# Performance work log

Hardware: AMD Instinct MI355X
Metric: run time of the kernel (lower is better)

## Reference

```python
import jax, jax.numpy as jnp
import numpy as np


def setup_inputs() -> dict:
    key = jax.random.key(0)
    x = jax.random.normal(key, (8192, 32768), dtype=jnp.float32)
    return {"x": x, "k": 64}


def reference(x, k):
    # ReLU then keep only top-k values per row; everything else zeroed.
    x_relu = jax.nn.relu(x)
    kk = min(k, x.shape[-1])
    vals, idx = jax.lax.top_k(x_relu, kk)            # [B, k]
    rows = jnp.arange(x.shape[0])[:, None]           # [B, 1]
    out = jnp.zeros_like(x).at[rows, idx].set(vals)
    return out
```

## Files before the change

### kernel.cpp

```cpp
#include <hip/hip_runtime.h>
#include <stdint.h>


#define NT   1024
#define NCOL 32768
#define VPT  8
#define NB   2048
#define REP  2
#define LISTCAP 2048

__global__ __launch_bounds__(NT) void topk_select_kernel(
        const float* __restrict__ x, const int* __restrict__ kptr,
        float* __restrict__ out)
{
    __shared__ uint32_t hist[REP][NB];
    __shared__ uint32_t tielist[LISTCAP];
    __shared__ int s_found, s_B, s_kth, s_neq, s_cnt, s_cut;

    const int tid  = threadIdx.x;
    const int lane = tid & 63;
    const int wave = tid >> 6;
    const size_t base = (size_t)blockIdx.x * NCOL;

    int k = *kptr;
    if (k > NCOL) k = NCOL;

    const uint4* xv = (const uint4*)(x + base);
    uint4*       ov = (uint4*)(out + base);

    if (k <= 0) {
        #pragma unroll
        for (int j = 0; j < VPT; ++j)
            ov[j * NT + tid] = make_uint4(0u, 0u, 0u, 0u);
        return;
    }

    uint4 va[VPT];
    #pragma unroll
    for (int j = 0; j < VPT; ++j) va[j] = xv[j * NT + tid];
    #pragma unroll
    for (int j = 0; j < VPT; ++j) {
        uint32_t* p = (uint32_t*)&va[j];
        #pragma unroll
        for (int c = 0; c < 4; ++c) {
            uint32_t u = p[c];
            p[c] = ((int)u > 0) ? u : 0u;
        }
    }

    int kth = k;
    uint32_t prefix = 0u;
    uint32_t thr = 0u;
    int n_eq = 0;
    bool done = false;

    #pragma unroll
    for (int round = 0; round < 3; ++round) {
        for (int i = tid; i < REP * NB; i += NT)
            ((uint32_t*)hist)[i] = 0u;
        __syncthreads();

        if (!done) {
            const int r = wave & (REP - 1);
            #pragma unroll
            for (int j = 0; j < VPT; ++j) {
                const uint32_t* p = (const uint32_t*)&va[j];
                #pragma unroll
                for (int c = 0; c < 4; ++c) {
                    uint32_t vv = p[c];
                    bool act; uint32_t bin;
                    if (round == 0)      { act = (vv != 0u);                          bin = vv >> 21; }
                    else if (round == 1) { act = (vv != 0u) && ((vv >> 21) == prefix); bin = (vv >> 10) & 0x7FFu; }
                    else                 { act = (vv != 0u) && ((vv >> 10) == prefix); bin = vv & 0x3FFu; }
                    if (act) atomicAdd(&hist[r][bin], 1u);
                }
            }
        }
        __syncthreads();

        if (wave == 0) {
            uint32_t s = 0;
            for (int i = 0; i < 32; ++i) {
                int b = lane * 32 + ((i + lane) & 31);
                #pragma unroll
                for (int r2 = 0; r2 < REP; ++r2) s += hist[r2][b];
            }
            uint32_t suf = s;
            #pragma unroll
            for (int d = 1; d < 64; d <<= 1) {
                uint32_t t2 = __shfl_down(suf, d);
                if (lane + d < 64) suf += t2;
            }
            uint32_t t1  = __shfl_down(suf, 1);
            uint32_t nxt = (lane == 63) ? 0u : t1;
            bool cond = (!done) && (suf >= (uint32_t)kth) && (nxt < (uint32_t)kth);
            unsigned long long mask = __ballot(cond);
            if (mask == 0ull) {
                if (lane == 0) s_found = 0;
            } else {
                int G = __ffsll(mask) - 1;
                uint32_t cntG = __shfl(nxt, G);
                uint32_t h2 = 0;
                if (lane < 32) {
                    int b = G * 32 + lane;
                    #pragma unroll
                    for (int r2 = 0; r2 < REP; ++r2) h2 += hist[r2][b];
                }
                uint32_t suf2 = h2;
                #pragma unroll
                for (int d = 1; d < 64; d <<= 1) {
                    uint32_t t2 = __shfl_down(suf2, d);
                    if (lane + d < 64) suf2 += t2;
                }
                uint32_t t3   = __shfl_down(suf2, 1);
                uint32_t nxt2 = (lane == 63) ? 0u : t3;
                uint32_t ts   = cntG + suf2;
                uint32_t tsn  = cntG + nxt2;
                bool cond2 = (lane < 32) && (ts >= (uint32_t)kth) && (tsn < (uint32_t)kth);
                unsigned long long m2 = __ballot(cond2);
                int l = __ffsll(m2) - 1;
                uint32_t ngt  = __shfl(tsn, l);
                uint32_t cbin = __shfl(suf2 - nxt2, l);
                if (lane == 0) {
                    s_found = 1;
                    s_B   = G * 32 + l;
                    s_kth = kth - (int)ngt;
                    s_neq = (int)cbin;
                }
            }
        }
        __syncthreads();

        if (!done) {
            if (!s_found) { done = true; thr = 0u; }
            else {
                int B = s_B;
                kth  = s_kth;
                n_eq = s_neq;
                if (round == 0)      prefix = (uint32_t)B;
                else if (round == 1) prefix = (prefix << 11) | (uint32_t)B;
                else                 thr    = (prefix << 10) | (uint32_t)B;
            }
        }
        __syncthreads();
    }

    if (tid == 0) s_cnt = 0;
    __syncthreads();
    const bool need_tb = (thr != 0u) && (n_eq != kth);
    if (need_tb) {
        #pragma unroll
        for (int j = 0; j < VPT; ++j) {
            const uint32_t* p = (const uint32_t*)&va[j];
            #pragma unroll
            for (int c = 0; c < 4; ++c) {
                if (p[c] == thr) {
                    int slot = atomicAdd(&s_cnt, 1);
                    if (slot < LISTCAP)
                        tielist[slot] = (uint32_t)(j * 4096 + tid * 4 + c);
                }
            }
        }
    }
    __syncthreads();
    if (need_tb && tid == 0) {
        int n = s_cnt; if (n > LISTCAP) n = LISTCAP;
        for (int i = 1; i < n; ++i) {
            uint32_t key = tielist[i]; int j2 = i - 1;
            while (j2 >= 0 && tielist[j2] > key) { tielist[j2 + 1] = tielist[j2]; --j2; }
            tielist[j2 + 1] = key;
        }
        s_cut = (kth >= 1 && kth <= n) ? (int)tielist[kth - 1] : 0x7FFFFFFF;
    }
    __syncthreads();
    const int idx_cut = need_tb ? s_cut : 0x7FFFFFFF;

    #pragma unroll
    for (int j = 0; j < VPT; ++j) {
        const uint32_t* p = (const uint32_t*)&va[j];
        uint4 o;
        uint32_t* q = (uint32_t*)&o;
        #pragma unroll
        for (int c = 0; c < 4; ++c) {
            uint32_t vv = p[c];
            int idx = j * 4096 + tid * 4 + c;
            bool keep = (vv > thr) || (thr != 0u && vv == thr && idx <= idx_cut);
            q[c] = keep ? vv : 0u;
        }
        ov[j * NT + tid] = o;
    }
}

extern "C" void kernel_launch(void* const* d_in, const int* in_sizes, int n_in,
                              void* d_out, int out_size, void* d_ws, size_t ws_size,
                              hipStream_t stream) {
    const float* x    = (const float*)d_in[0];
    const int*   kptr = (const int*)d_in[1];
    float*       out  = (float*)d_out;
    const int rows = in_sizes[0] / NCOL;
    topk_select_kernel<<<rows, NT, 0, stream>>>(x, kptr, out);
}
```

Before: 1.767 ms.

## Early-exit radix select via small candidate list with parallel rank selection

Stops the radix histogram rounds as soon as the bin holding the k-th value has at most 1024 elements. Those candidates (value plus reversed index) are gathered into shared memory and the exact k-th element is found with a parallel O(n^2) rank count. Histogram replicas are interleaved four-way to cut atomic contention, and output vectors with no value in the top bin are zero-stored early. The aim is to skip later histogram passes and the serial insertion-sort tie-break, at the cost of more branches and a quadratic rank loop over up to 1024 candidates.

```diff
diff --git a/kernel.cpp b/kernel.cpp
--- a/kernel.cpp
+++ b/kernel.cpp
@@ -2,20 +2,23 @@
 #include <stdint.h>
 
 
-#define NT   1024
-#define NCOL 32768
-#define VPT  8
-#define NB   2048
-#define REP  2
-#define LISTCAP 2048
+#define NT    1024
+#define NCOL  32768
+#define VPT   8
+#define NB    2048
+#define REP   4
+#define CAP   1024
 
 __global__ __launch_bounds__(NT) void topk_select_kernel(
         const float* __restrict__ x, const int* __restrict__ kptr,
         float* __restrict__ out)
 {
-    __shared__ uint32_t hist[REP][NB];
-    __shared__ uint32_t tielist[LISTCAP];
-    __shared__ int s_found, s_B, s_kth, s_neq, s_cnt, s_cut;
+    __shared__ uint32_t hist[NB][REP];
+    __shared__ uint32_t red[NB];
+    __shared__ uint64_t cand[CAP];
+    __shared__ int s_found, s_B, s_kth, s_cnt, s_nc;
+    __shared__ uint32_t s_thr;
+    __shared__ int s_cut;
 
     const int tid  = threadIdx.x;
     const int lane = tid & 63;
@@ -47,34 +50,76 @@
             p[c] = ((int)u > 0) ? u : 0u;
         }
     }
+    if (tid == 0) s_nc = 0;
 
     int kth = k;
-    uint32_t prefix = 0u;
+    uint32_t p11 = 0u, p22 = 0u, thrx = 0u, B3 = 0u;
+    uint32_t binfloor = 1u;
     uint32_t thr = 0u;
-    int n_eq = 0;
-    bool done = false;
-
-    #pragma unroll
-    for (int round = 0; round < 3; ++round) {
-        for (int i = tid; i < REP * NB; i += NT)
-            ((uint32_t*)hist)[i] = 0u;
-        __syncthreads();
-
-        if (!done) {
-            const int r = wave & (REP - 1);
-            #pragma unroll
-            for (int j = 0; j < VPT; ++j) {
-                const uint32_t* p = (const uint32_t*)&va[j];
-                #pragma unroll
-                for (int c = 0; c < 4; ++c) {
-                    uint32_t vv = p[c];
-                    bool act; uint32_t bin;
-                    if (round == 0)      { act = (vv != 0u);                          bin = vv >> 21; }
-                    else if (round == 1) { act = (vv != 0u) && ((vv >> 21) == prefix); bin = (vv >> 10) & 0x7FFu; }
-                    else                 { act = (vv != 0u) && ((vv >> 10) == prefix); bin = vv & 0x3FFu; }
-                    if (act) atomicAdd(&hist[r][bin], 1u);
-                }
-            }
+    int cut = -1;
+    int mode = 4;
+    const int rrep = tid & (REP - 1);
+
+    for (int round = 0; round < 4; ++round) {
+        {
+            uint4* h4 = (uint4*)&hist[0][0];
+            h4[tid]      = make_uint4(0u, 0u, 0u, 0u);
+            h4[tid + NT] = make_uint4(0u, 0u, 0u, 0u);
+        }
+        __syncthreads();
+
+        if (round == 0) {
+            #pragma unroll
+            for (int j = 0; j < VPT; ++j) {
+                const uint32_t* p = (const uint32_t*)&va[j];
+                #pragma unroll
+                for (int c = 0; c < 4; ++c) {
+                    uint32_t vv = p[c];
+                    if (vv) atomicAdd(&hist[vv >> 21][rrep], 1u);
+                }
+            }
+        } else if (round == 1) {
+            #pragma unroll
+            for (int j = 0; j < VPT; ++j) {
+                const uint32_t* p = (const uint32_t*)&va[j];
+                #pragma unroll
+                for (int c = 0; c < 4; ++c) {
+                    uint32_t vv = p[c];
+                    if (vv && (vv >> 21) == p11)
+                        atomicAdd(&hist[(vv >> 10) & 0x7FFu][rrep], 1u);
+                }
+            }
+        } else if (round == 2) {
+            #pragma unroll
+            for (int j = 0; j < VPT; ++j) {
+                const uint32_t* p = (const uint32_t*)&va[j];
+                #pragma unroll
+                for (int c = 0; c < 4; ++c) {
+                    uint32_t vv = p[c];
+                    if (vv && (vv >> 10) == p22)
+                        atomicAdd(&hist[vv & 0x3FFu][rrep], 1u);
+                }
+            }
+        } else {
+            #pragma unroll
+            for (int j = 0; j < VPT; ++j) {
+                const uint32_t* p = (const uint32_t*)&va[j];
+                #pragma unroll
+                for (int c = 0; c < 4; ++c) {
+                    uint32_t vv = p[c];
+                    int idx = j * 4096 + tid * 4 + c;
+                    if (vv == thrx)
+                        atomicAdd(&hist[(uint32_t)(32767 - idx) >> 4][rrep], 1u);
+                }
+            }
+        }
+        __syncthreads();
+
+        {
+            uint4 h0 = *(const uint4*)&hist[tid][0];
+            uint4 h1 = *(const uint4*)&hist[tid + NT][0];
+            red[tid]      = h0.x + h0.y + h0.z + h0.w;
+            red[tid + NT] = h1.x + h1.y + h1.z + h1.w;
         }
         __syncthreads();
 
@@ -82,8 +127,7 @@
             uint32_t s = 0;
             for (int i = 0; i < 32; ++i) {
                 int b = lane * 32 + ((i + lane) & 31);
-                #pragma unroll
-                for (int r2 = 0; r2 < REP; ++r2) s += hist[r2][b];
+                s += red[b];
             }
             uint32_t suf = s;
             #pragma unroll
@@ -93,7 +137,7 @@
             }
             uint32_t t1  = __shfl_down(suf, 1);
             uint32_t nxt = (lane == 63) ? 0u : t1;
-            bool cond = (!done) && (suf >= (uint32_t)kth) && (nxt < (uint32_t)kth);
+            bool cond = (suf >= (uint32_t)kth) && (nxt < (uint32_t)kth);
             unsigned long long mask = __ballot(cond);
             if (mask == 0ull) {
                 if (lane == 0) s_found = 0;
@@ -101,11 +145,7 @@
                 int G = __ffsll(mask) - 1;
                 uint32_t cntG = __shfl(nxt, G);
                 uint32_t h2 = 0;
-                if (lane < 32) {
-                    int b = G * 32 + lane;
-                    #pragma unroll
-                    for (int r2 = 0; r2 < REP; ++r2) h2 += hist[r2][b];
-                }
+                if (lane < 32) h2 = red[G * 32 + lane];
                 uint32_t suf2 = h2;
                 #pragma unroll
                 for (int d = 1; d < 64; d <<= 1) {
@@ -125,58 +165,131 @@
                     s_found = 1;
                     s_B   = G * 32 + l;
                     s_kth = kth - (int)ngt;
-                    s_neq = (int)cbin;
-                }
-            }
-        }
-        __syncthreads();
-
-        if (!done) {
-            if (!s_found) { done = true; thr = 0u; }
-            else {
-                int B = s_B;
-                kth  = s_kth;
-                n_eq = s_neq;
-                if (round == 0)      prefix = (uint32_t)B;
-                else if (round == 1) prefix = (prefix << 11) | (uint32_t)B;
-                else                 thr    = (prefix << 10) | (uint32_t)B;
-            }
-        }
-        __syncthreads();
-    }
-
-    if (tid == 0) s_cnt = 0;
-    __syncthreads();
-    const bool need_tb = (thr != 0u) && (n_eq != kth);
-    if (need_tb) {
-        #pragma unroll
-        for (int j = 0; j < VPT; ++j) {
-            const uint32_t* p = (const uint32_t*)&va[j];
-            #pragma unroll
-            for (int c = 0; c < 4; ++c) {
-                if (p[c] == thr) {
-                    int slot = atomicAdd(&s_cnt, 1);
-                    if (slot < LISTCAP)
-                        tielist[slot] = (uint32_t)(j * 4096 + tid * 4 + c);
-                }
-            }
-        }
-    }
-    __syncthreads();
-    if (need_tb && tid == 0) {
-        int n = s_cnt; if (n > LISTCAP) n = LISTCAP;
-        for (int i = 1; i < n; ++i) {
-            uint32_t key = tielist[i]; int j2 = i - 1;
-            while (j2 >= 0 && tielist[j2] > key) { tielist[j2 + 1] = tielist[j2]; --j2; }
-            tielist[j2 + 1] = key;
-        }
-        s_cut = (kth >= 1 && kth <= n) ? (int)tielist[kth - 1] : 0x7FFFFFFF;
-    }
-    __syncthreads();
-    const int idx_cut = need_tb ? s_cut : 0x7FFFFFFF;
-
+                    s_cnt = (int)cbin;
+                }
+            }
+        }
+        __syncthreads();
+
+        if (!s_found) { thr = 0u; cut = -1; mode = 4; break; }
+        kth = s_kth;
+        {
+            const int B = s_B, cnt = s_cnt;
+            if (round == 0) {
+                p11 = (uint32_t)B;
+                binfloor = p11 << 21;
+                if (cnt <= CAP) { mode = 0; break; }
+            } else if (round == 1) {
+                p22 = (p11 << 11) | (uint32_t)B;
+                if (cnt <= CAP) { mode = 1; break; }
+            } else if (round == 2) {
+                thrx = (p22 << 10) | (uint32_t)B;
+                if (cnt == kth) { thr = thrx; cut = 0x7FFFFFFF; mode = 4; break; }
+                if (cnt <= CAP) { mode = 2; break; }
+            } else {
+                B3 = (uint32_t)B;
+                mode = 3;
+            }
+        }
+    }
+
+    uint32_t defer = 0u;
     #pragma unroll
     for (int j = 0; j < VPT; ++j) {
+        const uint32_t* p = (const uint32_t*)&va[j];
+        bool anyhi = (p[0] >= binfloor) || (p[1] >= binfloor) ||
+                     (p[2] >= binfloor) || (p[3] >= binfloor);
+        if (anyhi) defer |= (1u << j);
+        else       ov[j * NT + tid] = make_uint4(0u, 0u, 0u, 0u);
+    }
+
+    if (mode != 4) {
+        if (mode == 0) {
+            #pragma unroll
+            for (int j = 0; j < VPT; ++j) {
+                if (!((defer >> j) & 1u)) continue;
+                const uint32_t* p = (const uint32_t*)&va[j];
+                #pragma unroll
+                for (int c = 0; c < 4; ++c) {
+                    uint32_t vv = p[c];
+                    if (vv && (vv >> 21) == p11) {
+                        int slot = atomicAdd(&s_nc, 1);
+                        int idx = j * 4096 + tid * 4 + c;
+                        if (slot < CAP)
+                            cand[slot] = ((uint64_t)vv << 32) | (uint32_t)(32767 - idx);
+                    }
+                }
+            }
+        } else if (mode == 1) {
+            #pragma unroll
+            for (int j = 0; j < VPT; ++j) {
+                if (!((defer >> j) & 1u)) continue;
+                const uint32_t* p = (const uint32_t*)&va[j];
+                #pragma unroll
+                for (int c = 0; c < 4; ++c) {
+                    uint32_t vv = p[c];
+                    if (vv && (vv >> 10) == p22) {
+                        int slot = atomicAdd(&s_nc, 1);
+                        int idx = j * 4096 + tid * 4 + c;
+                        if (slot < CAP)
+                            cand[slot] = ((uint64_t)vv << 32) | (uint32_t)(32767 - idx);
+                    }
+                }
+            }
+        } else if (mode == 2) {
+            #pragma unroll
+            for (int j = 0; j < VPT; ++j) {
+                if (!((defer >> j) & 1u)) continue;
+                const uint32_t* p = (const uint32_t*)&va[j];
+                #pragma unroll
+                for (int c = 0; c < 4; ++c) {
+                    uint32_t vv = p[c];
+                    if (vv == thrx) {
+                        int slot = atomicAdd(&s_nc, 1);
+                        int idx = j * 4096 + tid * 4 + c;
+                        if (slot < CAP)
+                            cand[slot] = ((uint64_t)vv << 32) | (uint32_t)(32767 - idx);
+                    }
+                }
+            }
+        } else {
+            #pragma unroll
+            for (int j = 0; j < VPT; ++j) {
+                if (!((defer >> j) & 1u)) continue;
+                const uint32_t* p = (const uint32_t*)&va[j];
+                #pragma unroll
+                for (int c = 0; c < 4; ++c) {
+                    uint32_t vv = p[c];
+                    int idx = j * 4096 + tid * 4 + c;
+                    if (vv == thrx && ((uint32_t)(32767 - idx) >> 4) == B3) {
+                        int slot = atomicAdd(&s_nc, 1);
+                        if (slot < CAP)
+                            cand[slot] = ((uint64_t)vv << 32) | (uint32_t)(32767 - idx);
+                    }
+                }
+            }
+        }
+        __syncthreads();
+
+        int n = s_nc; if (n > CAP) n = CAP;
+        if (tid < n) {
+            const uint64_t ci = cand[tid];
+            int rank = 0;
+            for (int j2 = 0; j2 < n; ++j2)
+                rank += (cand[j2] > ci) ? 1 : 0;
+            if (rank == kth - 1) {
+                s_thr = (uint32_t)(ci >> 32);
+                s_cut = 32767 - (int)(ci & 0xFFFFu);
+            }
+        }
+        __syncthreads();
+        thr = s_thr;
+        cut = s_cut;
+    }
+
+    #pragma unroll
+    for (int j = 0; j < VPT; ++j) {
+        if (!((defer >> j) & 1u)) continue;
         const uint32_t* p = (const uint32_t*)&va[j];
         uint4 o;
         uint32_t* q = (uint32_t*)&o;
@@ -184,7 +297,7 @@
         for (int c = 0; c < 4; ++c) {
             uint32_t vv = p[c];
             int idx = j * 4096 + tid * 4 + c;
-            bool keep = (vv > thr) || (thr != 0u && vv == thr && idx <= idx_cut);
+            bool keep = (vv > thr) || (thr != 0u && vv == thr && idx <= cut);
             q[c] = keep ? vv : 0u;
         }
         ov[j * NT + tid] = o;
```

Result: slower. 2.375 ms (+34.4%).
